# Kernel optimization log

Measured on AMD Instinct MI355X. Metric: run time of the kernel, lower is better.

The kernel has to match this reference:

```python
import jax, jax.numpy as jnp
import numpy as np

B, T, H, K = 64, 512, 768, 4  # batch, seq_len, bert hidden, tagset (BMES)


def setup_inputs() -> dict:
    key = jax.random.key(0)
    ks = jax.random.split(key, 6)
    return {
        "sentences": jax.random.normal(ks[0], (B, T, H), dtype=jnp.float32),
        "W": jax.random.normal(ks[1], (K, H), dtype=jnp.float32) * (1.0 / np.sqrt(H)),
        "b": jax.random.normal(ks[2], (K,), dtype=jnp.float32) * 0.01,
        "start_transitions": jax.random.uniform(ks[3], (K,), dtype=jnp.float32, minval=-0.1, maxval=0.1),
        "end_transitions": jax.random.uniform(ks[4], (K,), dtype=jnp.float32, minval=-0.1, maxval=0.1),
        "transitions": jax.random.uniform(ks[5], (K, K), dtype=jnp.float32, minval=-0.1, maxval=0.1),
    }


def reference(sentences, W, b, start_transitions, end_transitions, transitions):
    # hidden2tag linear projection: [B,T,H] @ [H,K] -> emissions [B,T,K]
    emissions = jnp.einsum("bth,kh->btk", sentences, W) + b

    # Viterbi forward pass (torchcrf decode with full mask)
    score0 = start_transitions + emissions[:, 0]  # [B,K]

    def step(score, emit_t):
        # score[b,i] + transitions[i,j] -> [B,K_prev,K_next]
        cand = score[:, :, None] + transitions[None, :, :]
        bp = jnp.argmax(cand, axis=1)            # [B,K] backpointer to prev tag
        new_score = jnp.max(cand, axis=1) + emit_t
        return new_score, bp

    emits_t = jnp.swapaxes(emissions[:, 1:], 0, 1)  # [T-1,B,K]
    last_score, history = jax.lax.scan(step, score0, emits_t)

    final = last_score + end_transitions            # [B,K]
    best_last = jnp.argmax(final, axis=-1)          # [B]

    # Backtrack: path[t] = history[t][b, path[t+1]] for t = T-2 .. 0
    def back(tag, bp_t):
        prev = jnp.take_along_axis(bp_t, tag[:, None], axis=1)[:, 0]
        return prev, prev

    _, prev_tags = jax.lax.scan(back, best_last, history, reverse=True)  # [T-1,B]
    tags = jnp.concatenate([prev_tags, best_last[None, :]], axis=0)      # [T,B]
    return jnp.transpose(tags).astype(jnp.int32)                         # [B,T]
```

## Files before the change

### kernel.cpp

```cpp
#include <hip/hip_runtime.h>
#include <stdint.h>

#define BB 64
#define TT 512
#define HH 768
#define KK 4

template <int CTRL>
__device__ __forceinline__ float dppf(float x) {
  return __int_as_float(__builtin_amdgcn_update_dpp(
      0, __float_as_int(x), CTRL, 0xF, 0xF, true));
}

__global__ __launch_bounds__(256) void emis_kernel(
    const float* __restrict__ sent, const float* __restrict__ W,
    const float* __restrict__ bias, float* __restrict__ emis) {
  const int lane  = threadIdx.x & 63;
  const int wave  = threadIdx.x >> 6;
  const int gwave = blockIdx.x * 4 + wave;

  const float4* Wv = (const float4*)W;
  float4 w[4][3];
#pragma unroll
  for (int k = 0; k < 4; ++k)
#pragma unroll
    for (int c = 0; c < 3; ++c) w[k][c] = Wv[k * 192 + c * 64 + lane];

  const float4 bb = ((const float4*)bias)[0];
  const float4* sv = (const float4*)sent;

  int row = gwave * 8;
  float4 x[3];
#pragma unroll
  for (int c = 0; c < 3; ++c) x[c] = sv[(size_t)row * 192 + c * 64 + lane];

#pragma unroll
  for (int it = 0; it < 8; ++it) {
    float4 xn[3];
    if (it < 7) {
#pragma unroll
      for (int c = 0; c < 3; ++c)
        xn[c] = sv[(size_t)(row + 1) * 192 + c * 64 + lane];
    }
    float a0 = 0.f, a1 = 0.f, a2 = 0.f, a3 = 0.f;
#pragma unroll
    for (int c = 0; c < 3; ++c) {
      a0 = fmaf(x[c].x, w[0][c].x, a0); a0 = fmaf(x[c].y, w[0][c].y, a0);
      a0 = fmaf(x[c].z, w[0][c].z, a0); a0 = fmaf(x[c].w, w[0][c].w, a0);
      a1 = fmaf(x[c].x, w[1][c].x, a1); a1 = fmaf(x[c].y, w[1][c].y, a1);
      a1 = fmaf(x[c].z, w[1][c].z, a1); a1 = fmaf(x[c].w, w[1][c].w, a1);
      a2 = fmaf(x[c].x, w[2][c].x, a2); a2 = fmaf(x[c].y, w[2][c].y, a2);
      a2 = fmaf(x[c].z, w[2][c].z, a2); a2 = fmaf(x[c].w, w[2][c].w, a2);
      a3 = fmaf(x[c].x, w[3][c].x, a3); a3 = fmaf(x[c].y, w[3][c].y, a3);
      a3 = fmaf(x[c].z, w[3][c].z, a3); a3 = fmaf(x[c].w, w[3][c].w, a3);
    }
#define RED16(a)                                                   \
    a += dppf<0x124>(a); a += dppf<0x128>(a);                      \
    a += dppf<0xB1>(a);  a += dppf<0x4E>(a);
    RED16(a0) RED16(a1) RED16(a2) RED16(a3)
#undef RED16
    a0 += __shfl_xor(a0, 16); a0 += __shfl_xor(a0, 32);
    a1 += __shfl_xor(a1, 16); a1 += __shfl_xor(a1, 32);
    a2 += __shfl_xor(a2, 16); a2 += __shfl_xor(a2, 32);
    a3 += __shfl_xor(a3, 16); a3 += __shfl_xor(a3, 32);
    if (lane == 0) {
      float4 o; o.x = a0 + bb.x; o.y = a1 + bb.y; o.z = a2 + bb.z; o.w = a3 + bb.w;
      ((float4*)emis)[row] = o;
    }
    row += 1;
#pragma unroll
    for (int c = 0; c < 3; ++c) x[c] = xn[c];
  }
}


__device__ __forceinline__ uint32_t map_compose(uint32_t f, uint32_t g) {
  uint32_t h = 0;
#pragma unroll
  for (int x = 0; x < 4; ++x) {
    uint32_t gx = (g >> (2 * x)) & 3u;
    uint32_t fx = (f >> (2 * gx)) & 3u;
    h |= fx << (2 * x);
  }
  return h;
}

__global__ __launch_bounds__(64) void viterbi_kernel(
    const float* __restrict__ emis, const float* __restrict__ trans,
    const float* __restrict__ startT, const float* __restrict__ endT,
    int* __restrict__ out) {
  const int b    = blockIdx.x;
  const int lane = threadIdx.x;
  const int j    = lane & 3;

  __shared__ float sc[TT][4];

  const float tr0 = trans[0 * 4 + j];
  const float tr1 = trans[1 * 4 + j];
  const float tr2 = trans[2 * 4 + j];
  const float tr3 = trans[3 * 4 + j];

  const float* eb = emis + b * (TT * KK);
  float s = startT[j] + eb[j];
  if (lane < 4) sc[0][j] = s;

  auto step = [&](int t, float e) {
    float v0 = dppf<0x00>(s);
    float v1 = dppf<0x55>(s);
    float v2 = dppf<0xAA>(s);
    float v3 = dppf<0xFF>(s);
    float c0 = v0 + tr0;
    float c1 = v1 + tr1;
    float c2 = v2 + tr2;
    float c3 = v3 + tr3;
    float m = fmaxf(fmaxf(c0, c1), fmaxf(c2, c3));
    s = m + e;
    if (lane < 4) sc[t][j] = s;
  };

  float ebuf[8];
#pragma unroll
  for (int q = 0; q < 8; ++q) ebuf[q] = eb[(1 + q) * 4 + j];

  for (int c = 0; c < 63; ++c) {
    float enext[8];
    const int base = 8 * c + 9;
#pragma unroll
    for (int q = 0; q < 8; ++q) {
      int tt = base + q; if (tt > 511) tt = 511;
      enext[q] = eb[tt * 4 + j];
    }
#pragma unroll
    for (int q = 0; q < 8; ++q) step(8 * c + 1 + q, ebuf[q]);
#pragma unroll
    for (int q = 0; q < 8; ++q) ebuf[q] = enext[q];
  }
#pragma unroll
  for (int q = 0; q < 7; ++q) step(505 + q, ebuf[q]);

  float f = s + endT[j];
  int best_last;
  {
    float f0 = dppf<0x00>(f);
    float f1 = dppf<0x55>(f);
    float f2 = dppf<0xAA>(f);
    float f3 = dppf<0xFF>(f);
    float bm = f0; int bi = 0;
    if (f1 > bm) { bm = f1; bi = 1; }
    if (f2 > bm) { bm = f2; bi = 2; }
    if (f3 > bm) { bm = f3; bi = 3; }
    best_last = bi;
  }

  __syncthreads();

  float t16[16];
#pragma unroll
  for (int i = 0; i < 16; ++i) t16[i] = trans[i];

  const int lo = 8 * lane + 1;
  uint32_t g[8];
  uint32_t A = 0xE4;
#pragma unroll
  for (int q = 7; q >= 0; --q) {
    const int sq = lo + q;
    uint32_t mq = 0xE4;
    if (sq <= 511) {
      const float4 pv = *((const float4*)sc[sq - 1]);
      mq = 0;
#pragma unroll
      for (int j2 = 0; j2 < 4; ++j2) {
        float c0 = pv.x + t16[0 * 4 + j2];
        float c1 = pv.y + t16[1 * 4 + j2];
        float c2 = pv.z + t16[2 * 4 + j2];
        float c3 = pv.w + t16[3 * 4 + j2];
        float bm = c0; uint32_t bi = 0;
        if (c1 > bm) { bm = c1; bi = 1; }
        if (c2 > bm) { bm = c2; bi = 2; }
        if (c3 > bm) { bm = c3; bi = 3; }
        mq |= bi << (2 * j2);
      }
    }
    g[q] = mq;
    A = map_compose(mq, A);
  }

  uint32_t V = A;
#pragma unroll
  for (int d = 1; d < 64; d <<= 1) {
    uint32_t o = __shfl_down(V, d);
    if (lane + d < 64) V = map_compose(V, o);
  }
  uint32_t S = __shfl_down(V, 1);
  if (lane == 63) S = 0xE4;

  int cur = (int)((S >> (2 * best_last)) & 3u);
  const int hi = min(lo + 7, 511);
  int* ob = out + b * TT;
  ob[hi] = cur;
#pragma unroll
  for (int q = 7; q >= 0; --q) {
    const int sq = lo + q;
    if (sq <= 511) {
      cur = (int)((g[q] >> (2 * cur)) & 3u);
      ob[sq - 1] = cur;
    }
  }
}

extern "C" void kernel_launch(void* const* d_in, const int* in_sizes, int n_in,
                              void* d_out, int out_size, void* d_ws, size_t ws_size,
                              hipStream_t stream) {
  const float* sent   = (const float*)d_in[0];
  const float* W      = (const float*)d_in[1];
  const float* bias   = (const float*)d_in[2];
  const float* startT = (const float*)d_in[3];
  const float* endT   = (const float*)d_in[4];
  const float* trans  = (const float*)d_in[5];
  float* emis = (float*)d_ws;
  int* outp   = (int*)d_out;

  emis_kernel<<<1024, 256, 0, stream>>>(sent, W, bias, emis);
  viterbi_kernel<<<BB, 64, 0, stream>>>(emis, trans, startT, endT, outp);
}
```

Measured before the change: 175.4 us.

## Record Viterbi backpointers in forward pass and stage emissions in LDS

The Viterbi kernel now stages each batch's emissions into shared memory with a coalesced float4 load, so the serial recurrence reads emissions from LDS instead of global memory. Backpointers are computed inline during the forward recurrence, packed 2 bits per step, and stored as words. The backtrack then only unpacks those words instead of recomputing argmaxes from stored scores. The emission kernel handles 4 rows per wave with twice as many blocks, trading per-wave prefetch depth for more parallelism. The argmax work adds a few ops to the serial critical path.

```diff
diff --git a/kernel.cpp b/kernel.cpp
--- a/kernel.cpp
+++ b/kernel.cpp
@@ -4,7 +4,6 @@
 #define BB 64
 #define TT 512
 #define HH 768
-#define KK 4
 
 template <int CTRL>
 __device__ __forceinline__ float dppf(float x) {
@@ -29,15 +28,15 @@
   const float4 bb = ((const float4*)bias)[0];
   const float4* sv = (const float4*)sent;
 
-  int row = gwave * 8;
+  int row = gwave * 4;
   float4 x[3];
 #pragma unroll
   for (int c = 0; c < 3; ++c) x[c] = sv[(size_t)row * 192 + c * 64 + lane];
 
 #pragma unroll
-  for (int it = 0; it < 8; ++it) {
+  for (int it = 0; it < 4; ++it) {
     float4 xn[3];
-    if (it < 7) {
+    if (it < 3) {
 #pragma unroll
       for (int c = 0; c < 3; ++c)
         xn[c] = sv[(size_t)(row + 1) * 192 + c * 64 + lane];
@@ -93,18 +92,31 @@
   const int lane = threadIdx.x;
   const int j    = lane & 3;
 
-  __shared__ float sc[TT][4];
+  __shared__ float4 em4[TT];
+  __shared__ uint32_t bpw[64][4];
+  float* em = (float*)em4;
+
+  const float4* ev = (const float4*)(emis + (size_t)b * (TT * 4));
+  float4 stg[8];
+#pragma unroll
+  for (int q = 0; q < 8; ++q) stg[q] = ev[q * 64 + lane];
+#pragma unroll
+  for (int q = 0; q < 8; ++q) em4[q * 64 + lane] = stg[q];
 
   const float tr0 = trans[0 * 4 + j];
   const float tr1 = trans[1 * 4 + j];
   const float tr2 = trans[2 * 4 + j];
   const float tr3 = trans[3 * 4 + j];
-
-  const float* eb = emis + b * (TT * KK);
-  float s = startT[j] + eb[j];
-  if (lane < 4) sc[0][j] = s;
-
-  auto step = [&](int t, float e) {
+  const float endj = endT[j];
+  const float s0j  = startT[j];
+
+  __syncthreads();
+
+  float s = s0j + em[j];
+  const bool store_lane = (lane < 4);
+
+  uint32_t acc;
+  auto step = [&](float e, int q) {
     float v0 = dppf<0x00>(s);
     float v1 = dppf<0x55>(s);
     float v2 = dppf<0xAA>(s);
@@ -113,14 +125,17 @@
     float c1 = v1 + tr1;
     float c2 = v2 + tr2;
     float c3 = v3 + tr3;
-    float m = fmaxf(fmaxf(c0, c1), fmaxf(c2, c3));
+    float m01 = fmaxf(c0, c1); uint32_t b01 = (c1 > c0) ? 1u : 0u;
+    float m23 = fmaxf(c2, c3); uint32_t b23 = (c3 > c2) ? 3u : 2u;
+    float m   = fmaxf(m01, m23);
+    uint32_t bi = (m23 > m01) ? b23 : b01;
     s = m + e;
-    if (lane < 4) sc[t][j] = s;
+    acc |= bi << (2 * q);
   };
 
   float ebuf[8];
 #pragma unroll
-  for (int q = 0; q < 8; ++q) ebuf[q] = eb[(1 + q) * 4 + j];
+  for (int q = 0; q < 8; ++q) ebuf[q] = em[(1 + q) * 4 + j];
 
   for (int c = 0; c < 63; ++c) {
     float enext[8];
@@ -128,17 +143,23 @@
 #pragma unroll
     for (int q = 0; q < 8; ++q) {
       int tt = base + q; if (tt > 511) tt = 511;
-      enext[q] = eb[tt * 4 + j];
-    }
-#pragma unroll
-    for (int q = 0; q < 8; ++q) step(8 * c + 1 + q, ebuf[q]);
+      enext[q] = em[tt * 4 + j];
+    }
+    acc = 0;
+#pragma unroll
+    for (int q = 0; q < 8; ++q) step(ebuf[q], q);
+    if (store_lane) bpw[c][j] = acc;
 #pragma unroll
     for (int q = 0; q < 8; ++q) ebuf[q] = enext[q];
   }
-#pragma unroll
-  for (int q = 0; q < 7; ++q) step(505 + q, ebuf[q]);
-
-  float f = s + endT[j];
+  {
+    acc = 0;
+#pragma unroll
+    for (int q = 0; q < 7; ++q) step(ebuf[q], q);
+    if (store_lane) bpw[63][j] = acc;
+  }
+
+  float f = s + endj;
   int best_last;
   {
     float f0 = dppf<0x00>(f);
@@ -154,9 +175,10 @@
 
   __syncthreads();
 
-  float t16[16];
-#pragma unroll
-  for (int i = 0; i < 16; ++i) t16[i] = trans[i];
+  const uint32_t w0 = bpw[lane][0];
+  const uint32_t w1 = bpw[lane][1];
+  const uint32_t w2 = bpw[lane][2];
+  const uint32_t w3 = bpw[lane][3];
 
   const int lo = 8 * lane + 1;
   uint32_t g[8];
@@ -166,20 +188,8 @@
     const int sq = lo + q;
     uint32_t mq = 0xE4;
     if (sq <= 511) {
-      const float4 pv = *((const float4*)sc[sq - 1]);
-      mq = 0;
-#pragma unroll
-      for (int j2 = 0; j2 < 4; ++j2) {
-        float c0 = pv.x + t16[0 * 4 + j2];
-        float c1 = pv.y + t16[1 * 4 + j2];
-        float c2 = pv.z + t16[2 * 4 + j2];
-        float c3 = pv.w + t16[3 * 4 + j2];
-        float bm = c0; uint32_t bi = 0;
-        if (c1 > bm) { bm = c1; bi = 1; }
-        if (c2 > bm) { bm = c2; bi = 2; }
-        if (c3 > bm) { bm = c3; bi = 3; }
-        mq |= bi << (2 * j2);
-      }
+      mq = ((w0 >> (2 * q)) & 3u) | (((w1 >> (2 * q)) & 3u) << 2) |
+           (((w2 >> (2 * q)) & 3u) << 4) | (((w3 >> (2 * q)) & 3u) << 6);
     }
     g[q] = mq;
     A = map_compose(mq, A);
@@ -220,6 +230,6 @@
   float* emis = (float*)d_ws;
   int* outp   = (int*)d_out;
 
-  emis_kernel<<<1024, 256, 0, stream>>>(sent, W, bias, emis);
+  emis_kernel<<<2048, 256, 0, stream>>>(sent, W, bias, emis);
   viterbi_kernel<<<BB, 64, 0, stream>>>(emis, trans, startT, endT, outp);
 }
```

New measurement: 179.5 us. +2.3%, slower.
